# Optimization experiments

Measured on AMD Instinct MI355X. Metric: run time of the kernel, lower is better.

Reference implementation:

```python
import jax, jax.numpy as jnp
import numpy as np

DM = 1024; NHEAD = 16; HD = 64; ROPE = 32; KVC = 256; QC = 384
NSEQ = 4; SPS = 256; S = NSEQ * SPS + 1; B = 2
SCALE = 1.0 / ((HD + ROPE) // 2)          # 1/48, per module
LAMBDA_INIT = 0.8 - 0.6 * float(np.exp(-0.3 * 0))  # depth=0 -> 0.2
EPS_RMS = 1.1920929e-07                   # torch default RMSNorm eps (finfo eps)
EPS_HEAD = 1e-5


def _make_freqs(sps):
    # precompute_freqs_cis with args.seq_len=SPS, qk_rope_dim=ROPE (YaRN correction)
    dim = ROPE // 2
    base = 10000.0
    factor = 40.0
    seq_len = SPS
    max_seqlen = seq_len * 4
    freqs = 1.0 / base ** (np.arange(0, dim, 2, dtype=np.float32) / dim)  # (dim//2,)

    def corr_dim(nr):
        return dim * np.log(seq_len / (nr * 2 * np.pi)) / (2 * np.log(base))

    low = max(int(np.floor(corr_dim(32.0))), 0)
    high = min(int(np.ceil(corr_dim(1.0))), dim - 1)
    if low == high:
        high = high + 0.001
    ramp = np.clip((np.arange(dim // 2, dtype=np.float32) - low) / (high - low), 0, 1)
    smooth = 1.0 - ramp
    freqs = freqs / factor * (1 - smooth) + freqs * smooth
    t = np.arange(max_seqlen, dtype=np.float32)
    ang = np.outer(t, freqs)  # (max_seqlen, dim//2)
    return np.cos(ang)[:sps].astype(np.float32), np.sin(ang)[:sps].astype(np.float32)


def _make_mask():
    # global-separator mask: column 0 attendable, rest = tiled causal-per-timestep blocks
    temp = np.triu(np.ones((SPS, SPS), dtype=np.int32), k=1)
    tiled = np.tile(temp, (NSEQ, NSEQ))
    full = np.ones((S, S), dtype=np.int32)
    full[:, 0] = 0
    full[1:, 1:] = tiled
    return full[None, None]  # (1,1,S,S), 1 = masked


def _rms(x, g, eps):
    return x * jax.lax.rsqrt(jnp.mean(x * x, axis=-1, keepdims=True) + eps) * g


def _rope(x, cos, sin):
    # x: (b, nseq, sps, 2*nhead, ROPE//2) -> rotate complex pairs in last dim
    b, ns, sps, h, d = x.shape
    xr = x.reshape(b, ns, sps, h, d // 2, 2)
    c = cos[None, None, :, None, :]
    s = sin[None, None, :, None, :]
    yr = xr[..., 0] * c - xr[..., 1] * s
    yi = xr[..., 0] * s + xr[..., 1] * c
    return jnp.stack([yr, yi], axis=-1).reshape(b, ns, sps, h, d)


def setup_inputs() -> dict:
    key = jax.random.key(0)
    ks = jax.random.split(key, 12)
    cos, sin = _make_freqs(SPS)
    inp = {
        "x": jax.random.normal(ks[0], (B, S, DM), dtype=jnp.float32),
        "mask": jnp.asarray(_make_mask()),
        "freqs_cos": jnp.asarray(cos),
        "freqs_sin": jnp.asarray(sin),
        "W_kv_down": jax.random.normal(ks[1], (DM, KVC + ROPE), dtype=jnp.float32) * 0.02,
        "W_q_down": jax.random.normal(ks[2], (DM, QC), dtype=jnp.float32) * 0.02,
        "W_kv_up": jax.random.normal(ks[3], (KVC, NHEAD * HD * 2), dtype=jnp.float32) * 0.02,
        "W_q_up": jax.random.normal(ks[4], (QC, NHEAD * (HD + ROPE)), dtype=jnp.float32) * 0.02,
        "W_o": jax.random.normal(ks[5], (NHEAD * HD, DM), dtype=jnp.float32) * 0.02,
        "g_kv_norm": jnp.ones((KVC,), dtype=jnp.float32),
        "g_q_norm": jnp.ones((QC,), dtype=jnp.float32),
        "g_head_norm": jnp.ones((HD,), dtype=jnp.float32),
        "lambda_q1": jax.random.normal(ks[6], (HD // 2,), dtype=jnp.float32) * 0.1,
        "lambda_k1": jax.random.normal(ks[7], (HD // 2,), dtype=jnp.float32) * 0.1,
        "lambda_q2": jax.random.normal(ks[8], (HD // 2,), dtype=jnp.float32) * 0.1,
        "lambda_k2": jax.random.normal(ks[9], (HD // 2,), dtype=jnp.float32) * 0.1,
    }
    return inp


def reference(x, mask, freqs_cos, freqs_sin, W_kv_down, W_q_down, W_kv_up, W_q_up,
              W_o, g_kv_norm, g_q_norm, g_head_norm,
              lambda_q1, lambda_k1, lambda_q2, lambda_k2):
    b, s, _ = x.shape
    sps = (s - 1) // NSEQ
    # KV latent compression
    ckv = x @ W_kv_down                                   # (b,S,KVC+ROPE)
    c_kv, k_rope = ckv[..., :KVC], ckv[..., KVC:]
    kv = _rms(c_kv, g_kv_norm, EPS_RMS) @ W_kv_up         # (b,S,NHEAD*2*HD)
    kv = kv.reshape(b, s, NHEAD, 2 * HD)
    k, v = kv[..., :HD], kv[..., HD:]
    k = k.reshape(b, s, NHEAD * 2, HD // 2)               # dual head-groups
    # Q latent compression
    qf = _rms(x @ W_q_down, g_q_norm, EPS_RMS) @ W_q_up
    qf = qf.reshape(b, s, NHEAD, HD + ROPE)
    q, q_rope = qf[..., :HD], qf[..., HD:]
    q = q.reshape(b, s, NHEAD * 2, HD // 2)
    # RoPE parts: shared k_rope tiled over heads, then split into dual groups
    k_rope = jnp.tile(k_rope[:, :, None, :], (1, 1, NHEAD, 1)).reshape(b, s, NHEAD * 2, ROPE // 2)
    q_rope = q_rope.reshape(b, s, NHEAD * 2, ROPE // 2)
    # rotate all positions except the global separator token (index 0)
    q_rot = _rope(q_rope[:, 1:].reshape(b, NSEQ, sps, NHEAD * 2, ROPE // 2), freqs_cos, freqs_sin)
    k_rot = _rope(k_rope[:, 1:].reshape(b, NSEQ, sps, NHEAD * 2, ROPE // 2), freqs_cos, freqs_sin)
    q_rope = jnp.concatenate([q_rope[:, :1], q_rot.reshape(b, s - 1, NHEAD * 2, ROPE // 2)], axis=1)
    k_rope = jnp.concatenate([k_rope[:, :1], k_rot.reshape(b, s - 1, NHEAD * 2, ROPE // 2)], axis=1)
    q = jnp.concatenate([q, q_rope], axis=-1).transpose(0, 2, 1, 3)  # (b,2H,S,48)
    k = jnp.concatenate([k, k_rope], axis=-1).transpose(0, 2, 1, 3)
    v = v.transpose(0, 2, 1, 3)                                      # (b,H,S,64)
    # cognitive (signed) softmax attention
    a = jnp.einsum('bhqd,bhkd->bhqk', q, k) * SCALE
    abs_a = jnp.where(mask == 1, -1e9, jnp.abs(a))
    a = jnp.sign(a) * jax.nn.softmax(abs_a, axis=-1)
    # differential combination of dual head-groups
    lam = (jnp.exp(jnp.sum(lambda_q1 * lambda_k1)) -
           jnp.exp(jnp.sum(lambda_q2 * lambda_k2)) + LAMBDA_INIT)
    a = a.reshape(b, NHEAD, 2, s, s)
    G = jnp.mean(a[:, :, 0], axis=-1, keepdims=True)
    a = a[:, :, 0] - lam * a[:, :, 1] + G * lam
    a = jnp.where(mask == 1, 0.0, a)
    out = jnp.einsum('bhqk,bhkd->bhqd', a, v).transpose(0, 2, 1, 3)  # (b,S,H,64)
    out = _rms(out, g_head_norm, EPS_HEAD)
    return out.reshape(b, s, NHEAD * HD) @ W_o
```

## Files before the change

### kernel.cpp

```cpp
#include <hip/hip_runtime.h>
#include <hip/hip_bf16.h>
#include <math.h>

#define NHEAD 16
#define SEQ 1025
#define BATCH 2
#define NH2 32
#define KSCALE (1.0f/48.0f)
#define EPS_RMS 1.1920929e-07f
#define EPS_HEAD 1e-05f
#define LAMBDA_INIT 0.2f
#define R_TOT (BATCH*SEQ)

typedef __attribute__((ext_vector_type(8))) short bf16x8;
typedef __attribute__((ext_vector_type(4))) float f32x4;
typedef __attribute__((ext_vector_type(4))) int  i32x4;

static __device__ __forceinline__ unsigned short f2bf(float x) {
    unsigned int u = __float_as_uint(x);
    unsigned int r = (u + 0x7fffu + ((u >> 16) & 1u)) >> 16;
    return (unsigned short)r;
}
static __device__ __forceinline__ float bf2f(unsigned short h) {
    return __uint_as_float(((unsigned int)h) << 16);
}
static __device__ __forceinline__ void split3(float v, unsigned short& h,
                                              unsigned short& m, unsigned short& l) {
    h = f2bf(v); float r1 = v - bf2f(h);
    m = f2bf(r1); float r2 = r1 - bf2f(m);
    l = f2bf(r2);
}
static __device__ __forceinline__ f32x4 MFMA(bf16x8 a, bf16x8 b, f32x4 c) {
    return __builtin_amdgcn_mfma_f32_16x16x32_bf16(a, b, c, 0, 0, 0);
}
static __device__ __forceinline__ void gl16(const unsigned short* g,
                                            unsigned short* l) {
    __builtin_amdgcn_global_load_lds(
        (const __attribute__((address_space(1))) void*)g,
        (__attribute__((address_space(3))) void*)l, 16, 0, 0);
}

__global__ __launch_bounds__(256) void conv_all(
    const float* __restrict__ x, const float* __restrict__ Wkvd,
    const float* __restrict__ Wqd, const float* __restrict__ Wkvu,
    const float* __restrict__ Wqu, const float* __restrict__ Wo,
    unsigned short* __restrict__ xh, unsigned short* __restrict__ xm,
    unsigned short* __restrict__ xl,
    unsigned short* __restrict__ Wdh, unsigned short* __restrict__ Wdm,
    unsigned short* __restrict__ Wdl,
    unsigned short* __restrict__ Wuh, unsigned short* __restrict__ Wum,
    unsigned short* __restrict__ Wul,
    unsigned short* __restrict__ Wqh, unsigned short* __restrict__ Wqm,
    unsigned short* __restrict__ Wql,
    unsigned short* __restrict__ Wo1)
{
    __shared__ float tile[32][33];
    int bid = blockIdx.x, tid = threadIdx.x;
    if (bid < 2050) {
        int i = bid * 1024 + tid * 4;
        f32x4 v = *(const f32x4*)(x + i);
#pragma unroll
        for (int j = 0; j < 4; ++j) {
            unsigned short h, m, l;
            split3(v[j], h, m, l);
            xh[i + j] = h; xm[i + j] = m; xl[i + j] = l;
        }
        return;
    }
    bid -= 2050;
    const float* W; unsigned short *Th, *Tm, *Tl; int K, N, gx;
    if (bid < 288)              { W = Wkvd; Th = Wdh; Tm = Wdm; Tl = Wdl; K = 1024; N = 288;  gx = 9;  }
    else if ((bid -= 288) < 384){ W = Wqd;  Th = Wdh + (size_t)288*1024; Tm = Wdm + (size_t)288*1024;
                                  Tl = Wdl + (size_t)288*1024; K = 1024; N = 384; gx = 12; }
    else if ((bid -= 384) < 512){ W = Wkvu; Th = Wuh; Tm = Wum; Tl = Wul; K = 256;  N = 2048; gx = 64; }
    else if ((bid -= 512) < 576){ W = Wqu;  Th = Wqh; Tm = Wqm; Tl = Wql; K = 384;  N = 1536; gx = 48; }
    else { bid -= 576;            W = Wo;   Th = Wo1; Tm = nullptr; Tl = nullptr; K = 1024; N = 1024; gx = 32; }

    int n0 = (bid % gx) * 32, k0 = (bid / gx) * 32;
    int tx = tid & 31, ty = tid >> 5;
    for (int kk = ty; kk < 32; kk += 8)
        tile[kk][tx] = W[(size_t)(k0 + kk) * N + n0 + tx];
    __syncthreads();
    for (int nn = ty; nn < 32; nn += 8) {
        int n = n0 + nn, k = k0 + tx;
        float v = tile[tx][nn];
        if (Tm) {
            unsigned short h, m, l;
            split3(v, h, m, l);
            Th[(size_t)n * K + k] = h;
            Tm[(size_t)n * K + k] = m;
            Tl[(size_t)n * K + k] = l;
        } else {
            Th[(size_t)n * K + k] = f2bf(v);
        }
    }
}

__device__ __forceinline__ void gemm3_body(
    unsigned short* LA, unsigned short* LB,
    const unsigned short* __restrict__ Ah, const unsigned short* __restrict__ Am,
    const unsigned short* __restrict__ Al,
    const unsigned short* __restrict__ Bh, const unsigned short* __restrict__ Bm,
    const unsigned short* __restrict__ Bl,
    float* __restrict__ C,
    unsigned short* __restrict__ D0, unsigned short* __restrict__ D1,
    unsigned short* __restrict__ D2, unsigned short* __restrict__ D3,
    const float* __restrict__ fcos, const float* __restrict__ fsin,
    int M, int N, int K, int kb, int ke, int epi, int bm, int bn)
{
    int tid = threadIdx.x;
    int wid = tid >> 6, lane = tid & 63;
    int la = lane & 15, lb = lane >> 4;
    int wr = (wid >> 1) * 64, wc = (wid & 1) * 64;
    int wr4 = wr >> 4, wc4 = wc >> 4;

    const unsigned short* APl[3] = {Ah, Am, Al};
    const unsigned short* BPl[3] = {Bh, Bm, Bl};

    int sg = tid >> 6, spos = tid & 63;
    int rowA0 = (sg << 4) + (spos & 15);
    int rowA1 = ((sg + 4) << 4) + (spos & 15);
    int kc = (spos >> 4) * 8;
    int wb = tid & 192;

    f32x4 acc[4][4];
#pragma unroll
    for (int m = 0; m < 4; ++m)
#pragma unroll
        for (int n = 0; n < 4; ++n) acc[m][n] = (f32x4){0.f, 0.f, 0.f, 0.f};

    auto LDF = [&](bf16x8* dst, const unsigned short* Lb, int p, int rb) {
#pragma unroll
        for (int q = 0; q < 4; ++q)
            dst[q] = *(const bf16x8*)&Lb[p * 4096 + ((rb + q) * 64 + lane) * 8];
    };
    auto MM = [&](bf16x8* av, bf16x8* bv) {
#pragma unroll
        for (int m = 0; m < 4; ++m)
#pragma unroll
            for (int n = 0; n < 4; ++n)
                acc[m][n] = MFMA(av[m], bv[n], acc[m][n]);
    };

    int grA0 = bm + rowA0; if (grA0 >= M) grA0 = M - 1;
    int grA1 = bm + rowA1; if (grA1 >= M) grA1 = M - 1;
    int gnB0 = bn + rowA0; if (gnB0 >= N) gnB0 = N - 1;
    int gnB1 = bn + rowA1; if (gnB1 >= N) gnB1 = N - 1;

    for (int k0 = kb; k0 < ke; k0 += 32) {
        __syncthreads();
#pragma unroll
        for (int p = 0; p < 3; ++p) {
            gl16(APl[p] + (size_t)grA0 * K + k0 + kc, &LA[p * 4096 + wb * 8]);
            gl16(APl[p] + (size_t)grA1 * K + k0 + kc, &LA[p * 4096 + (256 + wb) * 8]);
            gl16(BPl[p] + (size_t)gnB0 * K + k0 + kc, &LB[p * 4096 + wb * 8]);
            gl16(BPl[p] + (size_t)gnB1 * K + k0 + kc, &LB[p * 4096 + (256 + wb) * 8]);
        }
        __syncthreads();
        bf16x8 av[4], bv0[4], bv1[4], bvt[4];
        LDF(av, LA, 0, wr4); LDF(bv0, LB, 0, wc4);
        LDF(bv1, LB, 1, wc4); LDF(bvt, LB, 2, wc4);
        __builtin_amdgcn_s_setprio(1);
        MM(av, bv0); MM(av, bv1); MM(av, bvt);
        __builtin_amdgcn_s_setprio(0);
        LDF(bvt, LA, 1, wr4);
        __builtin_amdgcn_s_setprio(1);
        MM(bvt, bv0); MM(bvt, bv1);
        __builtin_amdgcn_s_setprio(0);
        LDF(bvt, LA, 2, wr4);
        __builtin_amdgcn_s_setprio(1);
        MM(bvt, bv0);
        __builtin_amdgcn_s_setprio(0);
    }

#pragma unroll
    for (int m = 0; m < 4; ++m)
#pragma unroll
        for (int n = 0; n < 4; ++n) {
            int gc = bn + wc + n * 16 + la;
#pragma unroll
            for (int r = 0; r < 4; ++r) {
                int gr = bm + wr + m * 16 + lb * 4 + r;
                float v = acc[m][n][r];
                if (epi == 0) {
                    if (gr < M && gc < N) C[(size_t)gr * N + gc] = v;
                } else if (epi == 1) {
                    if (gr < M) {
                        int b = gr / SEQ, s = gr - b * SEQ;
                        int h2 = gc >> 7, rem = gc & 127;
                        if (rem < 64) {
                            int H = 2 * h2 + (rem >> 5), d = rem & 31;
                            size_t idx = (((size_t)b * NH2 + H) * SEQ + s) * 48 + d;
                            unsigned short hh, mm2, ll;
                            split3(v, hh, mm2, ll);
                            D0[idx] = hh; D1[idx] = mm2; D2[idx] = ll;
                        } else {
                            D3[(((size_t)b * NHEAD + h2) * SEQ + s) * 64 + (rem - 64)] = f2bf(v);
                        }
                    }
                } else {
                    float pv = __shfl_xor(v, 1);
                    if (gr < M) {
                        int b = gr / SEQ, s = gr - b * SEQ;
                        int h2 = gc / 96, rem = gc - h2 * 96;
                        int H, d; float outv;
                        if (rem < 64) {
                            H = 2 * h2 + (rem >> 5); d = rem & 31; outv = v;
                        } else {
                            int dd = rem - 64;
                            int e = dd >> 4, j = (dd & 15) >> 1;
                            H = 2 * h2 + e; d = 32 + (dd & 15);
                            if (s != 0) {
                                int p = (s - 1) & 255;
                                float cc = fcos[p * 8 + j], sn = fsin[p * 8 + j];
                                outv = ((la & 1) == 0) ? (v * cc - pv * sn)
                                                       : (pv * sn + v * cc);
                            } else outv = v;
                        }
                        outv *= KSCALE;
                        size_t idx = (((size_t)b * NH2 + H) * SEQ + s) * 48 + d;
                        unsigned short hh, mm2, ll;
                        split3(outv, hh, mm2, ll);
                        D0[idx] = hh; D1[idx] = mm2; D2[idx] = ll;
                    }
                }
            }
        }
}

__global__ __launch_bounds__(256) void gemm_down(
    const unsigned short* __restrict__ Ah, const unsigned short* __restrict__ Am,
    const unsigned short* __restrict__ Al,
    const unsigned short* __restrict__ Bh, const unsigned short* __restrict__ Bm,
    const unsigned short* __restrict__ Bl,
    float* __restrict__ C0, float* __restrict__ C1)
{
    __shared__ __align__(16) unsigned short LA[3 * 4096];
    __shared__ __align__(16) unsigned short LB[3 * 4096];
    int z = blockIdx.z;
    gemm3_body(LA, LB, Ah, Am, Al, Bh, Bm, Bl, z ? C1 : C0,
               nullptr, nullptr, nullptr, nullptr, nullptr, nullptr,
               R_TOT, 672, 1024, z * 512, z * 512 + 512, 0,
               blockIdx.y * 128, blockIdx.x * 128);
}

__global__ __launch_bounds__(256) void gemm_up(
    const unsigned short* __restrict__ cnh, const unsigned short* __restrict__ cnm,
    const unsigned short* __restrict__ cnl,
    const unsigned short* __restrict__ Wuh, const unsigned short* __restrict__ Wum,
    const unsigned short* __restrict__ Wul,
    const unsigned short* __restrict__ qnh, const unsigned short* __restrict__ qnm,
    const unsigned short* __restrict__ qnl,
    const unsigned short* __restrict__ Wqh, const unsigned short* __restrict__ Wqm,
    const unsigned short* __restrict__ Wql,
    unsigned short* __restrict__ Kah, unsigned short* __restrict__ Kam,
    unsigned short* __restrict__ Kal, unsigned short* __restrict__ Va,
    unsigned short* __restrict__ Qah, unsigned short* __restrict__ Qam,
    unsigned short* __restrict__ Qal,
    const float* __restrict__ fcos, const float* __restrict__ fsin)
{
    __shared__ __align__(16) unsigned short LA[3 * 4096];
    __shared__ __align__(16) unsigned short LB[3 * 4096];
    bool isq = (blockIdx.x >= 16);
    if (!isq)
        gemm3_body(LA, LB, cnh, cnm, cnl, Wuh, Wum, Wul, nullptr,
                   Kah, Kam, Kal, Va, nullptr, nullptr,
                   R_TOT, 2048, 256, 0, 256, 1, blockIdx.y * 128, blockIdx.x * 128);
    else
        gemm3_body(LA, LB, qnh, qnm, qnl, Wqh, Wqm, Wql, nullptr,
                   Qah, Qam, Qal, nullptr, fcos, fsin,
                   R_TOT, 1536, 384, 0, 384, 2, blockIdx.y * 128, (blockIdx.x - 16) * 128);
}

__global__ __launch_bounds__(256) void gemm_out(
    const unsigned short* __restrict__ Ah, const unsigned short* __restrict__ Bh,
    float* __restrict__ C, int M, int N, int K)
{
    __shared__ __align__(16) unsigned short As[4096];
    __shared__ __align__(16) unsigned short Bs[4096];
    int tid = threadIdx.x;
    int wid = tid >> 6, lane = tid & 63;
    int la = lane & 15, lb = lane >> 4;
    int bm = blockIdx.y * 128, bn = blockIdx.x * 128;
    int wr = (wid >> 1) * 64, wc = (wid & 1) * 64;
    int wr4 = wr >> 4, wc4 = wc >> 4;

    int sg = tid >> 6, spos = tid & 63;
    int rowA0 = (sg << 4) + (spos & 15);
    int rowA1 = ((sg + 4) << 4) + (spos & 15);
    int kc = (spos >> 4) * 8;
    int wb = tid & 192;
    int grA0 = bm + rowA0; if (grA0 >= M) grA0 = M - 1;
    int grA1 = bm + rowA1; if (grA1 >= M) grA1 = M - 1;
    int gnB0 = bn + rowA0; if (gnB0 >= N) gnB0 = N - 1;
    int gnB1 = bn + rowA1; if (gnB1 >= N) gnB1 = N - 1;

    f32x4 acc[4][4];
#pragma unroll
    for (int m = 0; m < 4; ++m)
#pragma unroll
        for (int n = 0; n < 4; ++n) acc[m][n] = (f32x4){0.f, 0.f, 0.f, 0.f};
    for (int k0 = 0; k0 < K; k0 += 32) {
        __syncthreads();
        gl16(Ah + (size_t)grA0 * K + k0 + kc, &As[wb * 8]);
        gl16(Ah + (size_t)grA1 * K + k0 + kc, &As[(256 + wb) * 8]);
        gl16(Bh + (size_t)gnB0 * K + k0 + kc, &Bs[wb * 8]);
        gl16(Bh + (size_t)gnB1 * K + k0 + kc, &Bs[(256 + wb) * 8]);
        __syncthreads();
        bf16x8 a_[4], b_[4];
#pragma unroll
        for (int m = 0; m < 4; ++m) a_[m] = *(const bf16x8*)&As[((wr4 + m) * 64 + lane) * 8];
#pragma unroll
        for (int n = 0; n < 4; ++n) b_[n] = *(const bf16x8*)&Bs[((wc4 + n) * 64 + lane) * 8];
        __builtin_amdgcn_s_setprio(1);
#pragma unroll
        for (int m = 0; m < 4; ++m)
#pragma unroll
            for (int n = 0; n < 4; ++n) acc[m][n] = MFMA(a_[m], b_[n], acc[m][n]);
        __builtin_amdgcn_s_setprio(0);
    }
#pragma unroll
    for (int m = 0; m < 4; ++m)
#pragma unroll
        for (int n = 0; n < 4; ++n) {
            int gc = bn + wc + n * 16 + la;
            if (gc >= N) continue;
#pragma unroll
            for (int r = 0; r < 4; ++r) {
                int gr = bm + wr + m * 16 + lb * 4 + r;
                if (gr < M) C[(size_t)gr * N + gc] = acc[m][n][r];
            }
        }
}

__global__ __launch_bounds__(256) void k_rmsrope3(
    const float* __restrict__ ckvqd, const float* __restrict__ ckvqd2,
    unsigned short* __restrict__ cnh, unsigned short* __restrict__ cnm,
    unsigned short* __restrict__ cnl,
    unsigned short* __restrict__ qnh, unsigned short* __restrict__ qnm,
    unsigned short* __restrict__ qnl,
    unsigned short* __restrict__ Kah, unsigned short* __restrict__ Kam,
    unsigned short* __restrict__ Kal,
    const float* __restrict__ gkv, const float* __restrict__ gq,
    const float* __restrict__ fcos, const float* __restrict__ fsin)
{
    __shared__ float red[256];
    __shared__ float rot[32];
    int row = blockIdx.x, tid = threadIdx.x;
    int b = row / SEQ, s = row - b * SEQ;
    const float* cp  = ckvqd  + (size_t)row * 672;
    const float* cp2 = ckvqd2 + (size_t)row * 672;
    float c0 = cp[tid] + cp2[tid];
    float q0 = cp[288 + tid] + cp2[288 + tid];
    float q1 = (tid < 128) ? (cp[544 + tid] + cp2[544 + tid]) : 0.f;

    red[tid] = c0 * c0;
    __syncthreads();
    for (int o = 128; o; o >>= 1) { if (tid < o) red[tid] += red[tid + o]; __syncthreads(); }
    float inv1 = rsqrtf(red[0] * (1.f / 256.f) + EPS_RMS);
    __syncthreads();
    red[tid] = q0 * q0 + q1 * q1;
    __syncthreads();
    for (int o = 128; o; o >>= 1) { if (tid < o) red[tid] += red[tid + o]; __syncthreads(); }
    float inv2 = rsqrtf(red[0] * (1.f / 384.f) + EPS_RMS);

    unsigned short h, m, l;
    split3(c0 * inv1 * gkv[tid], h, m, l);
    size_t ci = (size_t)row * 256 + tid;
    cnh[ci] = h; cnm[ci] = m; cnl[ci] = l;

    split3(q0 * inv2 * gq[tid], h, m, l);
    size_t qi = (size_t)row * 384 + tid;
    qnh[qi] = h; qnm[qi] = m; qnl[qi] = l;
    if (tid < 128) {
        split3(q1 * inv2 * gq[256 + tid], h, m, l);
        qnh[qi + 256] = h; qnm[qi + 256] = m; qnl[qi + 256] = l;
    }

    if (tid < 16) {
        float r0 = cp[256 + 2 * tid] + cp2[256 + 2 * tid];
        float r1 = cp[256 + 2 * tid + 1] + cp2[256 + 2 * tid + 1];
        float o0, o1;
        if (s == 0) { o0 = r0; o1 = r1; }
        else {
            int p = (s - 1) & 255;
            int j = tid & 7;
            float cc = fcos[p * 8 + j], sn = fsin[p * 8 + j];
            o0 = r0 * cc - r1 * sn;
            o1 = r0 * sn + r1 * cc;
        }
        rot[2 * tid] = o0; rot[2 * tid + 1] = o1;
    }
    __syncthreads();
    for (int t = tid; t < 512; t += 256) {
        int H = t >> 4, dd = t & 15;
        int e = H & 1;
        split3(rot[e * 16 + dd], h, m, l);
        size_t idx = (((size_t)b * NH2 + H) * SEQ + s) * 48 + 32 + dd;
        Kah[idx] = h; Kam[idx] = m; Kal[idx] = l;
    }
}

__global__ __launch_bounds__(256, 2) void k_attn8(
    const unsigned short* __restrict__ Qah, const unsigned short* __restrict__ Qam,
    const unsigned short* __restrict__ Qal,
    const unsigned short* __restrict__ Kah, const unsigned short* __restrict__ Kam,
    const unsigned short* __restrict__ Kal,
    const unsigned short* __restrict__ Va, const float* __restrict__ ghead,
    const float* __restrict__ lq1, const float* __restrict__ lk1,
    const float* __restrict__ lq2, const float* __restrict__ lk2,
    unsigned short* __restrict__ attO)
{
    __shared__ __align__(16) unsigned short KS[6][3072];
    __shared__ __align__(16) unsigned short Vt[4096];
    __shared__ __align__(16) unsigned short Pl[4][1024];

    int bid0 = blockIdx.x;
    int bid = (bid0 & 7) * 68 + (bid0 >> 3);
    int rt = bid % 17;
    int bh = bid / 17;
    int h = bh & 15, b = bh >> 4;
    int tid = threadIdx.x, wid = tid >> 6, lane = tid & 63;
    int la = lane & 15, lb = lane >> 4;
    int r0 = rt * 64, r0w = r0 + wid * 16;

    float e1 = 0.f, e2 = 0.f;
    for (int i = 0; i < 32; ++i) { e1 = fmaf(lq1[i], lk1[i], e1); e2 = fmaf(lq2[i], lk2[i], e2); }
    float lam = __expf(e1) - __expf(e2) + LAMBDA_INIT;

    int pr[4];
#pragma unroll
    for (int g = 0; g < 4; ++g) {
        int r = r0w + lb * 4 + g;
        pr[g] = (r >= 1 && r < SEQ) ? ((r - 1) & 255) : -1;
    }
    int rA = r0w + la;
    int prA = (rA >= 1 && rA < SEQ) ? ((rA - 1) & 255) : -1;

    int prm = -1;
    for (int i = 0; i < 64; ++i) {
        int r = r0 + i;
        if (r >= 1 && r < SEQ) { int p = (r - 1) & 255; prm = p > prm ? p : prm; }
    }

    const size_t hb1 = ((size_t)(b * NH2 + 2 * h)) * SEQ * 48;
    const size_t hb2 = ((size_t)(b * NH2 + 2 * h + 1)) * SEQ * 48;
    const unsigned short* vp = Va + ((size_t)(b * NHEAD + h)) * SEQ * 64;
    const unsigned short* KP[6] = {Kah + hb1, Kam + hb1, Kal + hb1,
                                   Kah + hb2, Kam + hb2, Kal + hb2};

    int qrow = r0w + la; if (qrow > SEQ - 1) qrow = SEQ - 1;
    bf16x8 zf;
#pragma unroll
    for (int u = 0; u < 8; ++u) zf[u] = 0;
    bf16x8 q1[3][2], q2[3][2];
    {
        const unsigned short* QPl[3] = {Qah, Qam, Qal};
#pragma unroll
        for (int p = 0; p < 3; ++p)
#pragma unroll
            for (int f = 0; f < 2; ++f) {
                if (f == 0 || lb < 2) {
                    q1[p][f] = *(const bf16x8*)(QPl[p] + hb1 + (size_t)qrow * 48 + 32 * f + lb * 8);
                    q2[p][f] = *(const bf16x8*)(QPl[p] + hb2 + (size_t)qrow * 48 + 32 * f + lb * 8);
                } else { q1[p][f] = zf; q2[p][f] = zf; }
            }
    }

    int colA, uA, colB = 0, uB = 0;
    {
        int ci = tid;
        colA = ((ci >> 6) << 4) + (ci & 15);
        uA = (ci >> 4) & 3;
        if (tid < 128) {
            int c2 = tid;
            colB = ((c2 >> 5) << 4) + (c2 & 15);
            uB = 4 + ((c2 >> 4) & 1);
        }
    }
    int cv0 = tid >> 3, uv0 = tid & 7;
    int cv1 = (tid + 256) >> 3, uv1 = tid & 7;

    i32x4 preA[6], preB[6], vv[2];
    auto LOADT = [&](int c0n) {
        int gcA = c0n + colA; if (gcA > SEQ - 1) gcA = SEQ - 1;
#pragma unroll
        for (int p = 0; p < 6; ++p)
            preA[p] = *(const i32x4*)(KP[p] + (size_t)gcA * 48 + uA * 8);
        if (tid < 128) {
            int gcB = c0n + colB; if (gcB > SEQ - 1) gcB = SEQ - 1;
#pragma unroll
            for (int p = 0; p < 6; ++p)
                preB[p] = *(const i32x4*)(KP[p] + (size_t)gcB * 48 + uB * 8);
        }
        int gv0 = c0n + cv0; if (gv0 > SEQ - 1) gv0 = SEQ - 1;
        vv[0] = *(const i32x4*)(vp + (size_t)gv0 * 64 + uv0 * 8);
        int gv1 = c0n + cv1; if (gv1 > SEQ - 1) gv1 = SEQ - 1;
        vv[1] = *(const i32x4*)(vp + (size_t)gv1 * 64 + uv1 * 8);
    };
    auto WRITET = [&]() {
#pragma unroll
        for (int p = 0; p < 6; ++p)
            *(i32x4*)&KS[p][tid * 8] = preA[p];
        if (tid < 128) {
#pragma unroll
            for (int p = 0; p < 6; ++p)
                *(i32x4*)&KS[p][2048 + tid * 8] = preB[p];
        }
#pragma unroll
        for (int it = 0; it < 2; ++it) {
            int cv = it ? cv1 : cv0, uv = it ? uv1 : uv0;
            unsigned short tmp[8];
            *(i32x4*)tmp = vv[it];
#pragma unroll
            for (int j = 0; j < 8; ++j) {
                int d = uv * 8 + j;
                int g = ((d >> 4) << 1) + (cv >> 5);
                int pos = (((cv & 31) >> 3) << 4) + (d & 15);
                Vt[g * 512 + pos * 8 + (cv & 7)] = tmp[j];
            }
        }
    };

    f32x4 O1[4], O2[4], VS[4];
#pragma unroll
    for (int nd = 0; nd < 4; ++nd) {
        O1[nd] = (f32x4){0.f, 0.f, 0.f, 0.f};
        O2[nd] = (f32x4){0.f, 0.f, 0.f, 0.f};
        VS[nd] = (f32x4){0.f, 0.f, 0.f, 0.f};
    }
    float dA1[4] = {0.f, 0.f, 0.f, 0.f}, dA2[4] = {0.f, 0.f, 0.f, 0.f};
    float gsA[4] = {0.f, 0.f, 0.f, 0.f};
    f32x4 z = (f32x4){0.f, 0.f, 0.f, 0.f};

    LOADT(0);
    WRITET();
    __syncthreads();

    for (int j = 0; j <= 16; ++j) {
        bool need = (j == 16) ? (prm >= 255)
                              : (((j & 3) == 0) || (prm >= 64 * (j & 3) - 1));
        if (!need) continue;
        int c0 = j * 64;

        int nj = -1;
        for (int t2 = j + 1; t2 <= 16; ++t2) {
            bool nd2 = (t2 == 16) ? (prm >= 255)
                                  : (((t2 & 3) == 0) || (prm >= 64 * (t2 & 3) - 1));
            if (nd2) { nj = t2; break; }
        }
        if (nj >= 0) LOADT(nj * 64);

        f32x4 s1[4], s2[4];
        __builtin_amdgcn_s_setprio(1);
#pragma unroll
        for (int n = 0; n < 4; ++n) {
            int g0 = n * 512 + lane * 8;
            int g1 = 2048 + n * 256 + (lane & 31) * 8;
            bf16x8 kh0 = *(const bf16x8*)&KS[0][g0];
            bf16x8 kh1 = *(const bf16x8*)&KS[0][g1];
            bf16x8 km0 = *(const bf16x8*)&KS[1][g0];
            bf16x8 km1 = *(const bf16x8*)&KS[1][g1];
            bf16x8 kl0 = *(const bf16x8*)&KS[2][g0];
            bf16x8 kl1 = *(const bf16x8*)&KS[2][g1];
            f32x4 s = z;
            s = MFMA(q1[0][0], kh0, s); s = MFMA(q1[0][1], kh1, s);
            s = MFMA(q1[0][0], km0, s); s = MFMA(q1[0][1], km1, s);
            s = MFMA(q1[1][0], kh0, s); s = MFMA(q1[1][1], kh1, s);
            s = MFMA(q1[0][0], kl0, s); s = MFMA(q1[0][1], kl1, s);
            s = MFMA(q1[1][0], km0, s); s = MFMA(q1[1][1], km1, s);
            s = MFMA(q1[2][0], kh0, s); s = MFMA(q1[2][1], kh1, s);
            s1[n] = s;
        }
#pragma unroll
        for (int n = 0; n < 4; ++n) {
            int g0 = n * 512 + lane * 8;
            int g1 = 2048 + n * 256 + (lane & 31) * 8;
            bf16x8 kh0 = *(const bf16x8*)&KS[3][g0];
            bf16x8 kh1 = *(const bf16x8*)&KS[3][g1];
            bf16x8 km0 = *(const bf16x8*)&KS[4][g0];
            bf16x8 km1 = *(const bf16x8*)&KS[4][g1];
            bf16x8 kl0 = *(const bf16x8*)&KS[5][g0];
            bf16x8 kl1 = *(const bf16x8*)&KS[5][g1];
            f32x4 s = z;
            s = MFMA(q2[0][0], kh0, s); s = MFMA(q2[0][1], kh1, s);
            s = MFMA(q2[0][0], km0, s); s = MFMA(q2[0][1], km1, s);
            s = MFMA(q2[1][0], kh0, s); s = MFMA(q2[1][1], kh1, s);
            s = MFMA(q2[0][0], kl0, s); s = MFMA(q2[0][1], kl1, s);
            s = MFMA(q2[1][0], km0, s); s = MFMA(q2[1][1], km1, s);
            s = MFMA(q2[2][0], kh0, s); s = MFMA(q2[2][1], kh1, s);
            s2[n] = s;
        }
        __builtin_amdgcn_s_setprio(0);

        unsigned short p1v[4][4], p2v[4][4];
#pragma unroll
        for (int n = 0; n < 4; ++n) {
            int c = c0 + n * 16 + la;
            bool cz = (c == 0);
            int cm = (c - 1) & 255;
            bool cin = (c < SEQ);
#pragma unroll
            for (int g = 0; g < 4; ++g) {
                bool al = cz || (cin && cm <= pr[g]);
                float a = s1[n][g];
                float sa = __builtin_copysignf(__expf(fabsf(a)), a);
                sa = al ? sa : 0.f;
                p1v[n][g] = (unsigned short)((__float_as_uint(sa) + 0x8000u) >> 16);
                gsA[g] += sa;
                dA1[g] += fabsf(sa);
                float bb = s2[n][g];
                float sb = __builtin_copysignf(__expf(fabsf(bb)), bb);
                sb = al ? sb : 0.f;
                p2v[n][g] = (unsigned short)((__float_as_uint(sb) + 0x8000u) >> 16);
                dA2[g] += fabsf(sb);
            }
        }

#pragma unroll
        for (int n = 0; n < 4; ++n) {
            int pb = (n >> 1) * 512 + (((n & 1) << 1) + (la >> 3)) * 128 + (la & 7);
#pragma unroll
            for (int g = 0; g < 4; ++g)
                Pl[wid][pb + (lb * 4 + g) * 8] = p1v[n][g];
        }
        __asm__ volatile("s_waitcnt lgkmcnt(0)" ::: "memory");
        __builtin_amdgcn_sched_barrier(0);
        bf16x8 p1a0 = *(const bf16x8*)&Pl[wid][lane * 8];
        bf16x8 p1a1 = *(const bf16x8*)&Pl[wid][512 + lane * 8];
#pragma unroll
        for (int n = 0; n < 4; ++n) {
            int pb = (n >> 1) * 512 + (((n & 1) << 1) + (la >> 3)) * 128 + (la & 7);
#pragma unroll
            for (int g = 0; g < 4; ++g)
                Pl[wid][pb + (lb * 4 + g) * 8] = p2v[n][g];
        }
        __asm__ volatile("s_waitcnt lgkmcnt(0)" ::: "memory");
        __builtin_amdgcn_sched_barrier(0);
        bf16x8 p2a0 = *(const bf16x8*)&Pl[wid][lane * 8];
        bf16x8 p2a1 = *(const bf16x8*)&Pl[wid][512 + lane * 8];

        bf16x8 p0[2];
#pragma unroll
        for (int f = 0; f < 2; ++f)
#pragma unroll
            for (int jb = 0; jb < 8; ++jb) {
                int c = c0 + 32 * f + lb * 8 + jb;
                bool al = (c == 0) || (c < SEQ && ((c - 1) & 255) <= prA);
                p0[f][jb] = al ? (short)0x3F80 : (short)0;
            }

        __builtin_amdgcn_s_setprio(1);
#pragma unroll
        for (int nd = 0; nd < 4; ++nd) {
            bf16x8 vb0 = *(const bf16x8*)&Vt[(nd * 2) * 512 + lane * 8];
            bf16x8 vb1 = *(const bf16x8*)&Vt[(nd * 2 + 1) * 512 + lane * 8];
            O1[nd] = MFMA(p1a0, vb0, O1[nd]);
            O1[nd] = MFMA(p1a1, vb1, O1[nd]);
            O2[nd] = MFMA(p2a0, vb0, O2[nd]);
            O2[nd] = MFMA(p2a1, vb1, O2[nd]);
            VS[nd] = MFMA(p0[0], vb0, VS[nd]);
            VS[nd] = MFMA(p0[1], vb1, VS[nd]);
        }
        __builtin_amdgcn_s_setprio(0);

        if (nj >= 0) {
            __syncthreads();
            WRITET();
            __syncthreads();
        }
    }

#pragma unroll
    for (int off = 1; off < 16; off <<= 1) {
#pragma unroll
        for (int g = 0; g < 4; ++g) {
            dA1[g] += __shfl_xor(dA1[g], off);
            dA2[g] += __shfl_xor(dA2[g], off);
            gsA[g] += __shfl_xor(gsA[g], off);
        }
    }

    float i1[4], i2g[4], Gl[4];
#pragma unroll
    for (int g = 0; g < 4; ++g) {
        i1[g] = 1.f / dA1[g];
        i2g[g] = 1.f / dA2[g];
        Gl[g] = gsA[g] * i1[g] * (1.f / (float)SEQ) * lam;
    }
    f32x4 outv[4];
#pragma unroll
    for (int nd = 0; nd < 4; ++nd)
#pragma unroll
        for (int g = 0; g < 4; ++g)
            outv[nd][g] = O1[nd][g] * i1[g] - lam * i2g[g] * O2[nd][g] + Gl[g] * VS[nd][g];

    float ssq[4] = {0.f, 0.f, 0.f, 0.f};
#pragma unroll
    for (int nd = 0; nd < 4; ++nd)
#pragma unroll
        for (int g = 0; g < 4; ++g) ssq[g] += outv[nd][g] * outv[nd][g];
#pragma unroll
    for (int off = 1; off < 16; off <<= 1)
#pragma unroll
        for (int g = 0; g < 4; ++g) ssq[g] += __shfl_xor(ssq[g], off);
    float inv[4];
#pragma unroll
    for (int g = 0; g < 4; ++g) inv[g] = rsqrtf(ssq[g] * (1.f / 64.f) + EPS_HEAD);

#pragma unroll
    for (int nd = 0; nd < 4; ++nd) {
        int d = nd * 16 + la;
        float gv = ghead[d];
#pragma unroll
        for (int g = 0; g < 4; ++g) {
            int r = r0w + lb * 4 + g;
            if (r < SEQ)
                attO[(((size_t)b * SEQ + r) * NHEAD + h) * 64 + d] =
                    f2bf(outv[nd][g] * inv[g] * gv);
        }
    }
}

extern "C" void kernel_launch(void* const* d_in, const int* in_sizes, int n_in,
                              void* d_out, int out_size, void* d_ws, size_t ws_size,
                              hipStream_t stream)
{
    const float* x    = (const float*)d_in[0];
    const float* fcos = (const float*)d_in[2];
    const float* fsin = (const float*)d_in[3];
    const float* Wkvd = (const float*)d_in[4];
    const float* Wqd  = (const float*)d_in[5];
    const float* Wkvu = (const float*)d_in[6];
    const float* Wqu  = (const float*)d_in[7];
    const float* Wo   = (const float*)d_in[8];
    const float* gkv  = (const float*)d_in[9];
    const float* gq   = (const float*)d_in[10];
    const float* gh   = (const float*)d_in[11];
    const float* lq1  = (const float*)d_in[12];
    const float* lk1  = (const float*)d_in[13];
    const float* lq2  = (const float*)d_in[14];
    const float* lk2  = (const float*)d_in[15];
    float* out = (float*)d_out;

    const int R = R_TOT;
    char* base = (char*)d_ws;
    size_t off = 0;
    auto alloc = [&](size_t bytes) -> char* {
        char* p = base + off;
        off = (off + bytes + 255) & ~(size_t)255;
        return p;
    };
    const size_t KPL = (size_t)BATCH * NH2 * SEQ * 48 * 2;

    unsigned short* xh = (unsigned short*)alloc((size_t)R * 1024 * 2);
    unsigned short* xm = (unsigned short*)alloc((size_t)R * 1024 * 2);
    unsigned short* xl = (unsigned short*)alloc((size_t)R * 1024 * 2);
    unsigned short* attO = xh;
    unsigned short* Kah  = xm;

    float* ckvqd = (float*)alloc((size_t)R * 672 * 4);
    unsigned short* cnh = (unsigned short*)alloc((size_t)R * 256 * 2);
    unsigned short* cnm = (unsigned short*)alloc((size_t)R * 256 * 2);
    unsigned short* cnl = (unsigned short*)alloc((size_t)R * 256 * 2);
    unsigned short* qnh = (unsigned short*)alloc((size_t)R * 384 * 2);
    unsigned short* qnm = (unsigned short*)alloc((size_t)R * 384 * 2);
    unsigned short* qnl = (unsigned short*)alloc((size_t)R * 384 * 2);
    unsigned short* Kam = (unsigned short*)alloc(KPL);
    unsigned short* Kal = (unsigned short*)alloc(KPL);
    unsigned short* Qah = (unsigned short*)alloc(KPL);
    unsigned short* Qam = (unsigned short*)alloc(KPL);
    unsigned short* Qal = (unsigned short*)alloc(KPL);
    unsigned short* Va  = (unsigned short*)alloc((size_t)BATCH * NHEAD * SEQ * 64 * 2);
    unsigned short* Wdh = (unsigned short*)alloc((size_t)672 * 1024 * 2);
    unsigned short* Wdm = (unsigned short*)alloc((size_t)672 * 1024 * 2);
    unsigned short* Wdl = (unsigned short*)alloc((size_t)672 * 1024 * 2);
    unsigned short* Wuh = (unsigned short*)alloc((size_t)2048 * 256 * 2);
    unsigned short* Wum = (unsigned short*)alloc((size_t)2048 * 256 * 2);
    unsigned short* Wul = (unsigned short*)alloc((size_t)2048 * 256 * 2);
    unsigned short* Wqh = (unsigned short*)alloc((size_t)1536 * 384 * 2);
    unsigned short* Wqm = (unsigned short*)alloc((size_t)1536 * 384 * 2);
    unsigned short* Wql = (unsigned short*)alloc((size_t)1536 * 384 * 2);
    unsigned short* Wo1 = (unsigned short*)alloc((size_t)1024 * 1024 * 2);

    float* ckvqd2 = (float*)Qah;

    dim3 blk(256);
    conv_all<<<4834, blk, 0, stream>>>(x, Wkvd, Wqd, Wkvu, Wqu, Wo,
        xh, xm, xl, Wdh, Wdm, Wdl, Wuh, Wum, Wul, Wqh, Wqm, Wql, Wo1);
    gemm_down<<<dim3(6, 17, 2), blk, 0, stream>>>(xh, xm, xl, Wdh, Wdm, Wdl,
                                                  ckvqd, ckvqd2);
    k_rmsrope3<<<R, blk, 0, stream>>>(ckvqd, ckvqd2, cnh, cnm, cnl, qnh, qnm, qnl,
                                      Kah, Kam, Kal, gkv, gq, fcos, fsin);
    gemm_up<<<dim3(28, 17), blk, 0, stream>>>(cnh, cnm, cnl, Wuh, Wum, Wul,
        qnh, qnm, qnl, Wqh, Wqm, Wql, Kah, Kam, Kal, Va, Qah, Qam, Qal, fcos, fsin);
    k_attn8<<<544, blk, 0, stream>>>(Qah, Qam, Qal, Kah, Kam, Kal,
        Va, gh, lq1, lk1, lq2, lk2, attO);
    gemm_out<<<dim3(8, 17), blk, 0, stream>>>(attO, Wo1, out, R, 1024, 1024);
}
```

Before: 280.8 us.

## Pre-tile V in the up-projection epilogue into the attention LDS layout

The up-projection GEMM epilogue now writes V directly into 64-row tiles that match the transposed shared-memory layout the attention kernel uses. The attention kernel can then copy each V tile with plain vector loads and stores instead of scattering 2-byte elements into LDS one at a time. A memset zeroes the padded V buffer so the tail tile past the sequence end reads zeros. This adds scattered 2-byte global stores in the GEMM epilogue and an extra memset pass.

```diff
diff --git a/kernel.cpp b/kernel.cpp
--- a/kernel.cpp
+++ b/kernel.cpp
@@ -11,6 +11,7 @@
 #define EPS_HEAD 1e-05f
 #define LAMBDA_INIT 0.2f
 #define R_TOT (BATCH*SEQ)
+#define NVT 17
 
 typedef __attribute__((ext_vector_type(8))) short bf16x8;
 typedef __attribute__((ext_vector_type(4))) float f32x4;
@@ -195,7 +196,12 @@
                             split3(v, hh, mm2, ll);
                             D0[idx] = hh; D1[idx] = mm2; D2[idx] = ll;
                         } else {
-                            D3[(((size_t)b * NHEAD + h2) * SEQ + s) * 64 + (rem - 64)] = f2bf(v);
+                            int d = rem - 64;
+                            int cv = s & 63;
+                            int g = ((d >> 4) << 1) + (cv >> 5);
+                            int pos = (((cv & 31) >> 3) << 4) + (d & 15);
+                            D3[(((size_t)b * NHEAD + h2) * NVT + (s >> 6)) * 4096
+                               + g * 512 + pos * 8 + (cv & 7)] = f2bf(v);
                         }
                     }
                 } else {
@@ -401,7 +407,7 @@
     }
 }
 
-__global__ __launch_bounds__(256, 2) void k_attn8(
+__global__ __launch_bounds__(256, 2) void k_attn12(
     const unsigned short* __restrict__ Qah, const unsigned short* __restrict__ Qam,
     const unsigned short* __restrict__ Qal,
     const unsigned short* __restrict__ Kah, const unsigned short* __restrict__ Kam,
@@ -445,7 +451,7 @@
 
     const size_t hb1 = ((size_t)(b * NH2 + 2 * h)) * SEQ * 48;
     const size_t hb2 = ((size_t)(b * NH2 + 2 * h + 1)) * SEQ * 48;
-    const unsigned short* vp = Va + ((size_t)(b * NHEAD + h)) * SEQ * 64;
+    const unsigned short* vg = Va + ((size_t)(b * NHEAD + h)) * NVT * 4096;
     const unsigned short* KP[6] = {Kah + hb1, Kam + hb1, Kal + hb1,
                                    Kah + hb2, Kam + hb2, Kal + hb2};
 
@@ -478,8 +484,6 @@
             uB = 4 + ((c2 >> 4) & 1);
         }
     }
-    int cv0 = tid >> 3, uv0 = tid & 7;
-    int cv1 = (tid + 256) >> 3, uv1 = tid & 7;
 
     i32x4 preA[6], preB[6], vv[2];
     auto LOADT = [&](int c0n) {
@@ -493,10 +497,9 @@
             for (int p = 0; p < 6; ++p)
                 preB[p] = *(const i32x4*)(KP[p] + (size_t)gcB * 48 + uB * 8);
         }
-        int gv0 = c0n + cv0; if (gv0 > SEQ - 1) gv0 = SEQ - 1;
-        vv[0] = *(const i32x4*)(vp + (size_t)gv0 * 64 + uv0 * 8);
-        int gv1 = c0n + cv1; if (gv1 > SEQ - 1) gv1 = SEQ - 1;
-        vv[1] = *(const i32x4*)(vp + (size_t)gv1 * 64 + uv1 * 8);
+        const unsigned short* vt = vg + (size_t)(c0n >> 6) * 4096;
+        vv[0] = *(const i32x4*)(vt + tid * 8);
+        vv[1] = *(const i32x4*)(vt + 2048 + tid * 8);
     };
     auto WRITET = [&]() {
 #pragma unroll
@@ -507,19 +510,8 @@
             for (int p = 0; p < 6; ++p)
                 *(i32x4*)&KS[p][2048 + tid * 8] = preB[p];
         }
-#pragma unroll
-        for (int it = 0; it < 2; ++it) {
-            int cv = it ? cv1 : cv0, uv = it ? uv1 : uv0;
-            unsigned short tmp[8];
-            *(i32x4*)tmp = vv[it];
-#pragma unroll
-            for (int j = 0; j < 8; ++j) {
-                int d = uv * 8 + j;
-                int g = ((d >> 4) << 1) + (cv >> 5);
-                int pos = (((cv & 31) >> 3) << 4) + (d & 15);
-                Vt[g * 512 + pos * 8 + (cv & 7)] = tmp[j];
-            }
-        }
+        *(i32x4*)&Vt[tid * 8] = vv[0];
+        *(i32x4*)&Vt[2048 + tid * 8] = vv[1];
     };
 
     f32x4 O1[4], O2[4], VS[4];
@@ -752,6 +744,7 @@
         return p;
     };
     const size_t KPL = (size_t)BATCH * NH2 * SEQ * 48 * 2;
+    const size_t VAB = (size_t)BATCH * NHEAD * NVT * 4096 * 2;
 
     unsigned short* xh = (unsigned short*)alloc((size_t)R * 1024 * 2);
     unsigned short* xm = (unsigned short*)alloc((size_t)R * 1024 * 2);
@@ -771,7 +764,7 @@
     unsigned short* Qah = (unsigned short*)alloc(KPL);
     unsigned short* Qam = (unsigned short*)alloc(KPL);
     unsigned short* Qal = (unsigned short*)alloc(KPL);
-    unsigned short* Va  = (unsigned short*)alloc((size_t)BATCH * NHEAD * SEQ * 64 * 2);
+    unsigned short* Va  = (unsigned short*)alloc(VAB);
     unsigned short* Wdh = (unsigned short*)alloc((size_t)672 * 1024 * 2);
     unsigned short* Wdm = (unsigned short*)alloc((size_t)672 * 1024 * 2);
     unsigned short* Wdl = (unsigned short*)alloc((size_t)672 * 1024 * 2);
@@ -792,9 +785,10 @@
                                                   ckvqd, ckvqd2);
     k_rmsrope3<<<R, blk, 0, stream>>>(ckvqd, ckvqd2, cnh, cnm, cnl, qnh, qnm, qnl,
                                       Kah, Kam, Kal, gkv, gq, fcos, fsin);
+    hipMemsetAsync(Va, 0, VAB, stream);
     gemm_up<<<dim3(28, 17), blk, 0, stream>>>(cnh, cnm, cnl, Wuh, Wum, Wul,
         qnh, qnm, qnl, Wqh, Wqm, Wql, Kah, Kam, Kal, Va, Qah, Qam, Qal, fcos, fsin);
-    k_attn8<<<544, blk, 0, stream>>>(Qah, Qam, Qal, Kah, Kam, Kal,
+    k_attn12<<<544, blk, 0, stream>>>(Qah, Qam, Qal, Kah, Kam, Kal,
         Va, gh, lq1, lk1, lq2, lk2, attO);
     gemm_out<<<dim3(8, 17), blk, 0, stream>>>(attO, Wo1, out, R, 1024, 1024);
 }
```

Result: faster. 262.4 us (-6.5%).
